# Performance work log

Measured on AMD Instinct MI355X. Metric: run time of the kernel, lower is better.

Reference implementation:

```python
import jax, jax.numpy as jnp
import numpy as np


def setup_inputs() -> dict:
    key = jax.random.key(0)
    k1, k2 = jax.random.split(key)
    shape = (16, 64, 32, 28, 28)  # (b, c, t, h, w)
    x = jax.random.normal(k1, shape, dtype=jnp.float32)
    x_v = jax.random.normal(k2, shape, dtype=jnp.float32)
    return {"x": x, "x_v": x_v}


def reference(x, x_v):
    b, c, t, h, w = x.shape
    d = c * h * w
    # (b, t, d): flatten channel+spatial into feature dim per frame
    r_q = jnp.transpose(x, (0, 2, 1, 3, 4)).reshape(b, t, d)
    r_v = jnp.transpose(x_v, (0, 2, 1, 3, 4)).reshape(b, t, d)
    # (b, t, t) frame-frame similarity
    m_t = jnp.einsum('bqd,bkd->bqk', r_q, r_q)
    # NOTE: softmax over the BATCH axis (dim=0), faithful to the original
    m_t = jax.nn.softmax(m_t, axis=0)
    a_t = jnp.einsum('bqk,bkd->bqd', m_t, r_v)
    a = a_t.reshape(b, t, c, h, w).transpose(0, 2, 1, 3, 4)
    return a
```

## Files before the change

kernel.cpp:

```cpp
#include <hip/hip_runtime.h>

namespace {

constexpr int Tt = 32;
constexpr int Ss = 784;

using bf16x8 = __attribute__((ext_vector_type(8))) short;
using f32x4  = __attribute__((ext_vector_type(4))) float;

__device__ inline void cvt2(float a, float b, unsigned& h, unsigned& l) {
  const unsigned ha = __float_as_uint(a) >> 16;
  const unsigned hb = __float_as_uint(b) >> 16;
  const float ra = a - __uint_as_float(ha << 16);
  const float rb = b - __uint_as_float(hb << 16);
  const unsigned la = __float_as_uint(ra) >> 16;
  const unsigned lb = __float_as_uint(rb) >> 16;
  h = ha | (hb << 16);
  l = la | (lb << 16);
}

__device__ inline void gload16(const float* g, float* l) {
  __builtin_amdgcn_global_load_lds(
      (const __attribute__((address_space(1))) void*)g,
      (__attribute__((address_space(3))) void*)l, 16, 0, 0);
}

__global__ __launch_bounds__(256, 4) void gram_partial(const float* __restrict__ x,
                                                       float* __restrict__ part) {
  const int bc = blockIdx.x;
  const float* __restrict__ xb = x + (size_t)bc * (Tt * Ss);
  const int tid  = threadIdx.x;
  const int w    = tid >> 6;
  const int lane = tid & 63;
  const int col  = lane & 15;
  const int g    = lane >> 4;

  f32x4 d1[2][2], d2[2][2], d3[2][2];
#pragma unroll
  for (int i = 0; i < 2; ++i)
#pragma unroll
    for (int j = 0; j < 2; ++j) { d1[i][j] = 0.f; d2[i][j] = 0.f; d3[i][j] = 0.f; }

  const float* __restrict__ pa = xb + (size_t)col * Ss;
  const float* __restrict__ pb = xb + (size_t)(16 + col) * Ss;

  for (int ks = w; ks < 25; ks += 4) {
    const int s0 = ks * 32 + g * 8;
    uint4 ha = {0u,0u,0u,0u}, la = {0u,0u,0u,0u};
    uint4 hb = {0u,0u,0u,0u}, lb = {0u,0u,0u,0u};
    if (s0 < 784) {
      const float4 a0 = *reinterpret_cast<const float4*>(pa + s0);
      const float4 a1 = *reinterpret_cast<const float4*>(pa + s0 + 4);
      const float4 b0 = *reinterpret_cast<const float4*>(pb + s0);
      const float4 b1 = *reinterpret_cast<const float4*>(pb + s0 + 4);
      cvt2(a0.x, a0.y, ha.x, la.x);
      cvt2(a0.z, a0.w, ha.y, la.y);
      cvt2(a1.x, a1.y, ha.z, la.z);
      cvt2(a1.z, a1.w, ha.w, la.w);
      cvt2(b0.x, b0.y, hb.x, lb.x);
      cvt2(b0.z, b0.w, hb.y, lb.y);
      cvt2(b1.x, b1.y, hb.z, lb.z);
      cvt2(b1.z, b1.w, hb.w, lb.w);
    }
    const bf16x8 h0 = __builtin_bit_cast(bf16x8, ha);
    const bf16x8 l0 = __builtin_bit_cast(bf16x8, la);
    const bf16x8 h1 = __builtin_bit_cast(bf16x8, hb);
    const bf16x8 l1 = __builtin_bit_cast(bf16x8, lb);
    d1[0][0] = __builtin_amdgcn_mfma_f32_16x16x32_bf16(h0, h0, d1[0][0], 0, 0, 0);
    d1[0][1] = __builtin_amdgcn_mfma_f32_16x16x32_bf16(h0, h1, d1[0][1], 0, 0, 0);
    d1[1][0] = __builtin_amdgcn_mfma_f32_16x16x32_bf16(h1, h0, d1[1][0], 0, 0, 0);
    d1[1][1] = __builtin_amdgcn_mfma_f32_16x16x32_bf16(h1, h1, d1[1][1], 0, 0, 0);
    d2[0][0] = __builtin_amdgcn_mfma_f32_16x16x32_bf16(h0, l0, d2[0][0], 0, 0, 0);
    d2[0][1] = __builtin_amdgcn_mfma_f32_16x16x32_bf16(h0, l1, d2[0][1], 0, 0, 0);
    d2[1][0] = __builtin_amdgcn_mfma_f32_16x16x32_bf16(h1, l0, d2[1][0], 0, 0, 0);
    d2[1][1] = __builtin_amdgcn_mfma_f32_16x16x32_bf16(h1, l1, d2[1][1], 0, 0, 0);
    d3[0][0] = __builtin_amdgcn_mfma_f32_16x16x32_bf16(l0, h0, d3[0][0], 0, 0, 0);
    d3[0][1] = __builtin_amdgcn_mfma_f32_16x16x32_bf16(l0, h1, d3[0][1], 0, 0, 0);
    d3[1][0] = __builtin_amdgcn_mfma_f32_16x16x32_bf16(l1, h0, d3[1][0], 0, 0, 0);
    d3[1][1] = __builtin_amdgcn_mfma_f32_16x16x32_bf16(l1, h1, d3[1][1], 0, 0, 0);
  }

  __shared__ float mtmp[4 * 1056];
#pragma unroll
  for (int i = 0; i < 2; ++i)
#pragma unroll
    for (int j = 0; j < 2; ++j) {
      const f32x4 s4 = d1[i][j] + d2[i][j] + d3[i][j];
#pragma unroll
      for (int r = 0; r < 4; ++r) {
        const int row = i * 16 + g * 4 + r;
        const int cc  = j * 16 + col;
        mtmp[w * 1056 + row * 33 + cc] = s4[r];
      }
    }
  __syncthreads();

  const int e0 = tid * 4;
  float tmp[4];
#pragma unroll
  for (int u = 0; u < 4; ++u) {
    const int row = (e0 + u) >> 5;
    const int cc  = (e0 + u) & 31;
    float ss = 0.f;
#pragma unroll
    for (int ww = 0; ww < 4; ++ww) ss += mtmp[ww * 1056 + row * 33 + cc];
    tmp[u] = ss;
  }
  float4 o4;
  o4.x = tmp[0]; o4.y = tmp[1]; o4.z = tmp[2]; o4.w = tmp[3];
  *reinterpret_cast<float4*>(part + (size_t)bc * 1024 + e0) = o4;
}

__global__ __launch_bounds__(256) void reduce_c(const float* __restrict__ part,
                                                float* __restrict__ msum) {
  const int bid = blockIdx.x;
  const int b   = bid >> 2;
  const int e   = (bid & 3) * 256 + threadIdx.x;
  const float* __restrict__ p = part + (size_t)b * 64 * 1024 + e;
  float s0 = 0.f, s1 = 0.f, s2 = 0.f, s3 = 0.f;
#pragma unroll
  for (int c = 0; c < 64; c += 4) {
    s0 += p[(size_t)(c + 0) * 1024];
    s1 += p[(size_t)(c + 1) * 1024];
    s2 += p[(size_t)(c + 2) * 1024];
    s3 += p[(size_t)(c + 3) * 1024];
  }
  msum[b * 1024 + e] = (s0 + s1) + (s2 + s3);
}

__global__ __launch_bounds__(256) void softmax_b(const float* __restrict__ msum,
                                                 float* __restrict__ mq) {
  const int e = blockIdx.x * 256 + threadIdx.x;
  float l[16];
  float mx = -3.4e38f;
#pragma unroll
  for (int b = 0; b < 16; ++b) {
    l[b] = msum[b * 1024 + e];
    mx = fmaxf(mx, l[b]);
  }
  float s = 0.f;
#pragma unroll
  for (int b = 0; b < 16; ++b) {
    l[b] = expf(l[b] - mx);
    s += l[b];
  }
  const float inv = 1.f / s;
#pragma unroll
  for (int b = 0; b < 16; ++b) mq[b * 1024 + e] = l[b] * inv;
}

__global__ __launch_bounds__(256, 4) void pv(const float* __restrict__ xv,
                                             const float* __restrict__ mq,
                                             float* __restrict__ out) {
  const int bc = blockIdx.x;
  const int b  = bc >> 6;
  const float* __restrict__ xvb = xv + (size_t)bc * (Tt * Ss);
  float* __restrict__ ob        = out + (size_t)bc * (Tt * Ss);

  const int tid  = threadIdx.x;
  const int w    = tid >> 6;
  const int lane = tid & 63;
  const int col  = lane & 15;
  const int g    = lane >> 4;

  __shared__ float lds[2][32 * 128];

  bf16x8 mh[2], ml[2];
#pragma unroll
  for (int qf = 0; qf < 2; ++qf) {
    const float* mp = mq + b * 1024 + (qf * 16 + col) * 32 + g * 8;
    const float4 ma = *reinterpret_cast<const float4*>(mp);
    const float4 mb = *reinterpret_cast<const float4*>(mp + 4);
    uint4 h, l;
    cvt2(ma.x, ma.y, h.x, l.x);
    cvt2(ma.z, ma.w, h.y, l.y);
    cvt2(mb.x, mb.y, h.z, l.z);
    cvt2(mb.z, mb.w, h.w, l.w);
    mh[qf] = __builtin_bit_cast(bf16x8, h);
    ml[qf] = __builtin_bit_cast(bf16x8, l);
  }

  auto stage = [&](int buf, int ch) {
    const int off = ch * 128;
#pragma unroll
    for (int round = 0; round < 4; ++round) {
      const int v   = round * 256 + tid;
      const int row = v >> 5;
      const int c4  = v & 31;
      gload16(xvb + row * Ss + off + c4 * 4,
              &lds[buf][(round * 256 + w * 64) * 4]);
    }
  };

  stage(0, 0);
  stage(1, 1);

#pragma unroll
  for (int ch = 0; ch < 6; ++ch) {
    if (ch == 0 || ch == 5) {
      asm volatile("s_waitcnt vmcnt(4)" ::: "memory");
    } else {
      asm volatile("s_waitcnt vmcnt(8)" ::: "memory");
    }
    __builtin_amdgcn_sched_barrier(0);
    __builtin_amdgcn_s_barrier();

    const float* __restrict__ lbuf = lds[ch & 1];
    const int off = ch * 128;
#pragma unroll
    for (int fi = 0; fi < 2; ++fi) {
      const int sf = 2 * w + fi;
      float f8[8];
#pragma unroll
      for (int j = 0; j < 8; ++j)
        f8[j] = lbuf[(8 * g + j) * 128 + sf * 16 + col];
      uint4 hh, lv;
      cvt2(f8[0], f8[1], hh.x, lv.x);
      cvt2(f8[2], f8[3], hh.y, lv.y);
      cvt2(f8[4], f8[5], hh.z, lv.z);
      cvt2(f8[6], f8[7], hh.w, lv.w);
      const bf16x8 vh = __builtin_bit_cast(bf16x8, hh);
      const bf16x8 vl = __builtin_bit_cast(bf16x8, lv);
      const int s0 = off + sf * 16;
#pragma unroll
      for (int qf = 0; qf < 2; ++qf) {
        f32x4 d = {0.f, 0.f, 0.f, 0.f};
        d = __builtin_amdgcn_mfma_f32_16x16x32_bf16(vl, mh[qf], d, 0, 0, 0);
        d = __builtin_amdgcn_mfma_f32_16x16x32_bf16(vh, ml[qf], d, 0, 0, 0);
        d = __builtin_amdgcn_mfma_f32_16x16x32_bf16(vh, mh[qf], d, 0, 0, 0);
        float4 o4;
        o4.x = d[0]; o4.y = d[1]; o4.z = d[2]; o4.w = d[3];
        *reinterpret_cast<float4*>(ob + (size_t)(qf * 16 + col) * Ss + s0 + 4 * g) = o4;
      }
    }
    asm volatile("s_waitcnt lgkmcnt(0)" ::: "memory");
    __builtin_amdgcn_sched_barrier(0);
    __builtin_amdgcn_s_barrier();
    if (ch < 4) stage(ch & 1, ch + 2);
  }

  if (w == 3) {
    float f8[8];
#pragma unroll
    for (int j = 0; j < 8; ++j)
      f8[j] = xvb[(size_t)(8 * g + j) * Ss + 768 + col];
    uint4 hh, lv;
    cvt2(f8[0], f8[1], hh.x, lv.x);
    cvt2(f8[2], f8[3], hh.y, lv.y);
    cvt2(f8[4], f8[5], hh.z, lv.z);
    cvt2(f8[6], f8[7], hh.w, lv.w);
    const bf16x8 vh = __builtin_bit_cast(bf16x8, hh);
    const bf16x8 vl = __builtin_bit_cast(bf16x8, lv);
#pragma unroll
    for (int qf = 0; qf < 2; ++qf) {
      f32x4 d = {0.f, 0.f, 0.f, 0.f};
      d = __builtin_amdgcn_mfma_f32_16x16x32_bf16(vl, mh[qf], d, 0, 0, 0);
      d = __builtin_amdgcn_mfma_f32_16x16x32_bf16(vh, ml[qf], d, 0, 0, 0);
      d = __builtin_amdgcn_mfma_f32_16x16x32_bf16(vh, mh[qf], d, 0, 0, 0);
      float4 o4;
      o4.x = d[0]; o4.y = d[1]; o4.z = d[2]; o4.w = d[3];
      *reinterpret_cast<float4*>(ob + (size_t)(qf * 16 + col) * Ss + 768 + 4 * g) = o4;
    }
  }
}

}

extern "C" void kernel_launch(void* const* d_in, const int* in_sizes, int n_in,
                              void* d_out, int out_size, void* d_ws, size_t ws_size,
                              hipStream_t stream) {
  const float* x  = (const float*)d_in[0];
  const float* xv = (const float*)d_in[1];
  float* out = (float*)d_out;

  float* part = (float*)d_ws;
  float* msum = part + 1024 * 1024;
  float* mq   = msum + 16 * 1024;

  gram_partial<<<dim3(1024), dim3(256), 0, stream>>>(x, part);
  reduce_c<<<dim3(64), dim3(256), 0, stream>>>(part, msum);
  softmax_b<<<dim3(4), dim3(256), 0, stream>>>(msum, mq);
  pv<<<dim3(1024), dim3(256), 0, stream>>>(xv, mq, out);
}
```

Baseline: 73.43 us.

## Restructure pv kernel to 8 waves with per-wave triple-buffered LDS staging

The pv kernel moves from 4 waves to 8 waves per block. Each wave now owns a private triple-buffered LDS region and streams its own 16-column strips of xv, which removes the block-wide barriers between chunks. The vmcnt waits are retuned for three loads in flight per wave, and the leftover tail strip moves to wave 0. This trades block-level synchronization for more waves per block and more outstanding loads, at the cost of higher LDS use per block, which may limit occupancy.

```diff
diff --git a/kernel.cpp b/kernel.cpp
--- a/kernel.cpp
+++ b/kernel.cpp
@@ -149,7 +149,7 @@
   for (int b = 0; b < 16; ++b) mq[b * 1024 + e] = l[b] * inv;
 }
 
-__global__ __launch_bounds__(256, 4) void pv(const float* __restrict__ xv,
+__global__ __launch_bounds__(512, 4) void pv(const float* __restrict__ xv,
                                              const float* __restrict__ mq,
                                              float* __restrict__ out) {
   const int bc = blockIdx.x;
@@ -163,7 +163,8 @@
   const int col  = lane & 15;
   const int g    = lane >> 4;
 
-  __shared__ float lds[2][32 * 128];
+  __shared__ float lds[8 * 3 * 512];
+  float* __restrict__ wbase = &lds[w * 3 * 512];
 
   bf16x8 mh[2], ml[2];
 #pragma unroll
@@ -180,66 +181,64 @@
     ml[qf] = __builtin_bit_cast(bf16x8, l);
   }
 
-  auto stage = [&](int buf, int ch) {
-    const int off = ch * 128;
-#pragma unroll
-    for (int round = 0; round < 4; ++round) {
-      const int v   = round * 256 + tid;
-      const int row = v >> 5;
-      const int c4  = v & 31;
-      gload16(xvb + row * Ss + off + c4 * 4,
-              &lds[buf][(round * 256 + w * 64) * 4]);
+  auto stage = [&](int t, int sf) {
+#pragma unroll
+    for (int p = 0; p < 2; ++p) {
+      const int row = p * 16 + (lane >> 2);
+      gload16(xvb + (size_t)row * Ss + sf * 16 + (lane & 3) * 4,
+              wbase + t * 512 + p * 256);
     }
   };
 
-  stage(0, 0);
-  stage(1, 1);
-
-#pragma unroll
-  for (int ch = 0; ch < 6; ++ch) {
-    if (ch == 0 || ch == 5) {
-      asm volatile("s_waitcnt vmcnt(4)" ::: "memory");
-    } else {
-      asm volatile("s_waitcnt vmcnt(8)" ::: "memory");
-    }
+  auto frag = [&](int t, int sf) {
+    float f8[8];
+#pragma unroll
+    for (int j = 0; j < 8; ++j)
+      f8[j] = wbase[t * 512 + (8 * g + j) * 16 + col];
+    uint4 hh, lv;
+    cvt2(f8[0], f8[1], hh.x, lv.x);
+    cvt2(f8[2], f8[3], hh.y, lv.y);
+    cvt2(f8[4], f8[5], hh.z, lv.z);
+    cvt2(f8[6], f8[7], hh.w, lv.w);
+    const bf16x8 vh = __builtin_bit_cast(bf16x8, hh);
+    const bf16x8 vl = __builtin_bit_cast(bf16x8, lv);
+    const int s0 = sf * 16;
+#pragma unroll
+    for (int qf = 0; qf < 2; ++qf) {
+      f32x4 d = {0.f, 0.f, 0.f, 0.f};
+      d = __builtin_amdgcn_mfma_f32_16x16x32_bf16(vl, mh[qf], d, 0, 0, 0);
+      d = __builtin_amdgcn_mfma_f32_16x16x32_bf16(vh, ml[qf], d, 0, 0, 0);
+      d = __builtin_amdgcn_mfma_f32_16x16x32_bf16(vh, mh[qf], d, 0, 0, 0);
+      float4 o4;
+      o4.x = d[0]; o4.y = d[1]; o4.z = d[2]; o4.w = d[3];
+      *reinterpret_cast<float4*>(ob + (size_t)(qf * 16 + col) * Ss + s0 + 4 * g) = o4;
+    }
+  };
+
+  stage(0, w);
+  stage(1, w + 8);
+  stage(2, w + 16);
+
+#pragma unroll
+  for (int i = 0; i < 6; ++i) {
+    if (i == 0)      asm volatile("s_waitcnt vmcnt(4)" ::: "memory");
+    else if (i == 1) asm volatile("s_waitcnt vmcnt(6)" ::: "memory");
+    else if (i == 2) asm volatile("s_waitcnt vmcnt(8)" ::: "memory");
+    else if (i == 3) asm volatile("s_waitcnt vmcnt(8)" ::: "memory");
+    else if (i == 4) asm volatile("s_waitcnt vmcnt(6)" ::: "memory");
+    else             asm volatile("s_waitcnt vmcnt(4)" ::: "memory");
     __builtin_amdgcn_sched_barrier(0);
-    __builtin_amdgcn_s_barrier();
-
-    const float* __restrict__ lbuf = lds[ch & 1];
-    const int off = ch * 128;
-#pragma unroll
-    for (int fi = 0; fi < 2; ++fi) {
-      const int sf = 2 * w + fi;
-      float f8[8];
-#pragma unroll
-      for (int j = 0; j < 8; ++j)
-        f8[j] = lbuf[(8 * g + j) * 128 + sf * 16 + col];
-      uint4 hh, lv;
-      cvt2(f8[0], f8[1], hh.x, lv.x);
-      cvt2(f8[2], f8[3], hh.y, lv.y);
-      cvt2(f8[4], f8[5], hh.z, lv.z);
-      cvt2(f8[6], f8[7], hh.w, lv.w);
-      const bf16x8 vh = __builtin_bit_cast(bf16x8, hh);
-      const bf16x8 vl = __builtin_bit_cast(bf16x8, lv);
-      const int s0 = off + sf * 16;
-#pragma unroll
-      for (int qf = 0; qf < 2; ++qf) {
-        f32x4 d = {0.f, 0.f, 0.f, 0.f};
-        d = __builtin_amdgcn_mfma_f32_16x16x32_bf16(vl, mh[qf], d, 0, 0, 0);
-        d = __builtin_amdgcn_mfma_f32_16x16x32_bf16(vh, ml[qf], d, 0, 0, 0);
-        d = __builtin_amdgcn_mfma_f32_16x16x32_bf16(vh, mh[qf], d, 0, 0, 0);
-        float4 o4;
-        o4.x = d[0]; o4.y = d[1]; o4.z = d[2]; o4.w = d[3];
-        *reinterpret_cast<float4*>(ob + (size_t)(qf * 16 + col) * Ss + s0 + 4 * g) = o4;
-      }
-    }
-    asm volatile("s_waitcnt lgkmcnt(0)" ::: "memory");
-    __builtin_amdgcn_sched_barrier(0);
-    __builtin_amdgcn_s_barrier();
-    if (ch < 4) stage(ch & 1, ch + 2);
-  }
-
-  if (w == 3) {
+
+    frag(i % 3, w + 8 * i);
+
+    if (i + 3 < 6) {
+      asm volatile("s_waitcnt lgkmcnt(0)" ::: "memory");
+      __builtin_amdgcn_sched_barrier(0);
+      stage(i % 3, w + 8 * (i + 3));
+    }
+  }
+
+  if (w == 0) {
     float f8[8];
 #pragma unroll
     for (int j = 0; j < 8; ++j)
@@ -280,5 +279,5 @@
   gram_partial<<<dim3(1024), dim3(256), 0, stream>>>(x, part);
   reduce_c<<<dim3(64), dim3(256), 0, stream>>>(part, msum);
   softmax_b<<<dim3(4), dim3(256), 0, stream>>>(msum, mq);
-  pv<<<dim3(1024), dim3(256), 0, stream>>>(xv, mq, out);
-}
+  pv<<<dim3(1024), dim3(512), 0, stream>>>(xv, mq, out);
+}
```

Result: slower. 84.47 us (+15.0%).
